# Performance work log

Measured on AMD Instinct MI355X. Metric: run time of the kernel, lower is better.

## Reference

```python
import jax, jax.numpy as jnp
import numpy as np

N = 100000; E = 1600000
X_DIM = 128; Y_DIM = 32; H_DIM = 128; R_DIM = 128; Z_DIM = 64
TAU = 1.0; KEEP = 0.1  # dropout p=0.9 -> keep prob 0.1


def spmm(edge_index, edge_weight, h):
    # out[row] += w * h[col]  (sparse [N,N] @ dense [N,D])
    row, col = edge_index[0], edge_index[1]
    return jax.ops.segment_sum(h[col] * edge_weight[:, None], row, num_segments=N)


def setup_inputs() -> dict:
    key = jax.random.key(0)
    ks = jax.random.split(key, 32)
    p = lambda k, shp: (0.02 * jax.random.normal(k, shp)).astype(jnp.float32)
    inp = {
        'x': jax.random.normal(ks[0], (N, X_DIM), dtype=jnp.float32),
        'y_': jax.random.uniform(ks[1], (N, Y_DIM), dtype=jnp.float32),
        'edge_index': jax.random.randint(ks[2], (2, E), 0, N, dtype=jnp.int32),
        'edge_weight': jax.random.uniform(ks[3], (E,), dtype=jnp.float32),
        'non_label': jax.random.bernoulli(ks[4], 0.5, (N,)),
        # inverted dropout mask, torch semantics: keep w.p. 0.1, scale by 1/0.1
        'dropout_mask': (jax.random.bernoulli(ks[5], KEEP, (N, X_DIM)).astype(jnp.float32) / KEEP),
        'u_gumbel': jax.random.uniform(ks[6], (N, Y_DIM), dtype=jnp.float32),
        'z_eps': jax.random.normal(ks[7], (Z_DIM,), dtype=jnp.float32),
        # x_to_yu (2-layer spmm GCN)
        'Wg1': p(ks[8], (X_DIM, H_DIM)), 'bg1': jnp.zeros((H_DIM,), jnp.float32),
        'Wg2': p(ks[9], (H_DIM, Y_DIM)), 'bg2': jnp.zeros((Y_DIM,), jnp.float32),
        # GSNN_Encoder
        'W_xy': p(ks[10], (H_DIM + Y_DIM, R_DIM)), 'b_xy': jnp.zeros((R_DIM,), jnp.float32),
        'W_hr': p(ks[11], (R_DIM, R_DIM)), 'b_hr': jnp.zeros((R_DIM,), jnp.float32),
        # R_to_MuSigma
        'W_rh': p(ks[12], (R_DIM, R_DIM)), 'b_rh': jnp.zeros((R_DIM,), jnp.float32),
        'W_mu': p(ks[13], (R_DIM, Z_DIM)), 'b_mu': jnp.zeros((Z_DIM,), jnp.float32),
        'W_sig': p(ks[14], (R_DIM, Z_DIM)), 'b_sig': jnp.zeros((Z_DIM,), jnp.float32),
        # GSNN_Decoder
        'W_xh': p(ks[15], (X_DIM, H_DIM)), 'b_xh': jnp.zeros((H_DIM,), jnp.float32),
        'W_h2': p(ks[16], (H_DIM + Z_DIM, H_DIM + Z_DIM)), 'b_h2': jnp.zeros((H_DIM + Z_DIM,), jnp.float32),
        'W_hy': p(ks[17], (H_DIM + Z_DIM, Y_DIM)), 'b_hy': jnp.zeros((Y_DIM,), jnp.float32),
    }
    return inp


def reference(x, y_, edge_index, edge_weight, non_label, dropout_mask, u_gumbel, z_eps,
              Wg1, bg1, Wg2, bg2, W_xy, b_xy, W_hr, b_hr,
              W_rh, b_rh, W_mu, b_mu, W_sig, b_sig,
              W_xh, b_xh, W_h2, b_h2, W_hy, b_hy):
    # ---- x_to_yu: 2-layer spmm GCN -> (y_encode [N,Y], y_embedding [N,H]) ----
    h_emb = jax.nn.relu(spmm(edge_index, edge_weight, x) @ Wg1 + bg1)
    y_encode = spmm(edge_index, edge_weight, h_emb) @ Wg2 + bg2
    # ---- gumbel_softmax(hard=True, tau=1) at non-labelled nodes ----
    g = -jnp.log(-jnp.log(u_gumbel + 1e-10) + 1e-10)
    soft = jax.nn.softmax((y_encode + g) / TAU, axis=-1)
    hard = jax.nn.one_hot(jnp.argmax(soft, axis=-1), Y_DIM, dtype=soft.dtype)
    y_gumbel = hard + soft - jax.lax.stop_gradient(soft)  # straight-through
    y = jnp.where(non_label[:, None], y_gumbel, y_)
    # ---- GSNN_Encoder (adj unused, matching original) ----
    h_enc = jax.nn.relu(jnp.concatenate([h_emb, y], axis=1) @ W_xy + b_xy)
    r_nodes = h_enc @ W_hr + b_hr
    r_graph = jnp.mean(r_nodes, axis=0)  # readout [R]
    # ---- R_to_MuSigma + rsample ----
    hr = jax.nn.relu(r_graph @ W_rh + b_rh)
    mu = hr @ W_mu + b_mu
    sigma = 0.1 + 0.9 * jax.nn.sigmoid(hr @ W_sig + b_sig)
    z = mu + sigma * z_eps  # Normal.rsample
    # ---- GSNN_Decoder ----
    xd = x * dropout_mask
    h = jax.nn.relu(xd @ W_xh + b_xh)
    h = jnp.concatenate([h, jnp.broadcast_to(z, (h.shape[0], Z_DIM))], axis=1)
    h = h / (jnp.linalg.norm(h, axis=1, keepdims=True) + 1e-06)
    h = jax.nn.relu(spmm(edge_index, edge_weight, h) @ W_h2 + b_h2)
    y_pred = spmm(edge_index, edge_weight, h) @ W_hy + b_hy
    return y_pred
```

## Files before the change

kernel.cpp:

```cpp
#include <hip/hip_runtime.h>
#include <hip/hip_bf16.h>

#define NN 100000
#define EE 1600000

typedef unsigned short u16;
typedef unsigned int   u32;
typedef short short8 __attribute__((ext_vector_type(8)));
typedef float v4f    __attribute__((ext_vector_type(4)));
typedef u32 u32x2    __attribute__((ext_vector_type(2)));

__device__ __forceinline__ float b2f(u16 h){ u32 u = ((u32)h) << 16; return __builtin_bit_cast(float, u); }
__device__ __forceinline__ float lo2f(u32 u){ return __builtin_bit_cast(float, u << 16); }
__device__ __forceinline__ float hi2f(u32 u){ return __builtin_bit_cast(float, u & 0xffff0000u); }
__device__ __forceinline__ u16   f2b(float f){ __hip_bfloat16 h = __float2bfloat16(f); return __builtin_bit_cast(u16, h); }
__device__ __forceinline__ float ldx(const void* p, long i, int fm){
  return fm ? ((const float*)p)[i] : b2f(((const u16*)p)[i]);
}
__device__ __forceinline__ float i2f(int v){ return __builtin_bit_cast(float, v); }

__global__ void k_detect(const void* __restrict__ x, const void* __restrict__ nonlab,
                         int* __restrict__ flags){
  __shared__ int s_bad, s_ni, s_nf, s_nb;
  int t = threadIdx.x;
  if (t == 0){ s_bad = 0; s_ni = 0; s_nf = 0; s_nb = 0; }
  __syncthreads();
  u32 w = ((const u32*)x)[t];
  u32 lo = w & 0xffffu, ex = (lo >> 7) & 0xffu;
  if (lo != 0u && (ex < 100u || ex > 140u)) atomicAdd(&s_bad, 1);
  if (t < 64){
    u32 v = ((const u32*)nonlab)[t];
    if (v > 1u) atomicAdd(&s_ni, 1);
    if (v != 0u && v != 0x3F800000u) atomicAdd(&s_nf, 1);
  }
  if (t < 128){
    u16 h = ((const u16*)nonlab)[t];
    if (h != 0 && h != 0x3F80) atomicAdd(&s_nb, 1);
  }
  __syncthreads();
  if (t == 0){
    flags[0] = (s_bad > 32) ? 1 : 0;
    flags[1] = (s_ni == 0) ? 1 : ((s_nf == 0) ? 3 : ((s_nb == 0) ? 2 : 0));
  }
}

#define PW_G1 0
#define PW_G2 16384
#define PW_XY 20480
#define PW_XH 40960
#define PW_H2 57344
#define PW_HY 94208
#define PW_TOT 100352
#define PB_G1 0
#define PB_XY 128
#define PB_XH 256
#define PB_H2 384
#define PB_ZERO 576
#define PB_HY 704
#define PB_TOT 736

__global__ __launch_bounds__(256) void k_pack(const void* W0, const void* W1, const void* W2,
                      const void* W3, const void* W4, const void* W5,
                      const void* b0, const void* b1, const void* b2, const void* b3, const void* b4,
                      u16* __restrict__ Wp, float* __restrict__ bp, const int* __restrict__ flags){
  int e = blockIdx.x * 256 + threadIdx.x;
  int fm = flags[0];
  if (e < PW_TOT){
    const void* src; int off, DOUT;
    if      (e < PW_G2){ src = W0; off = PW_G1; DOUT = 128; }
    else if (e < PW_XY){ src = W1; off = PW_G2; DOUT = 32; }
    else if (e < PW_XH){ src = W2; off = PW_XY; DOUT = 128; }
    else if (e < PW_H2){ src = W3; off = PW_XH; DOUT = 128; }
    else if (e < PW_HY){ src = W4; off = PW_H2; DOUT = 192; }
    else               { src = W5; off = PW_HY; DOUT = 32; }
    int local = e - off;
    int k = local / DOUT, col = local - k * DOUT;
    u16 v = fm ? f2b(((const float*)src)[local]) : ((const u16*)src)[local];
    Wp[off + ((k >> 3) * DOUT + col) * 8 + (k & 7)] = v;
  }
  int eb = e - PW_TOT;
  if (eb >= 0 && eb < PB_TOT){
    float v = 0.f;
    if      (eb < 128) v = ldx(b0, eb, fm);
    else if (eb < 256) v = ldx(b1, eb - 128, fm);
    else if (eb < 384) v = ldx(b2, eb - 256, fm);
    else if (eb < 576) v = ldx(b3, eb - 384, fm);
    else if (eb < 704) v = 0.f;
    else               v = ldx(b4, eb - 704, fm);
    bp[eb] = v;
  }
}

#define BSH 9
#define NBK 196
#define CAP 16384

__global__ __launch_bounds__(256) void k_binA(const int* __restrict__ ei, const void* __restrict__ ew,
                      int* __restrict__ bcnt, int2* __restrict__ stage,
                      const int* __restrict__ flags){
  __shared__ int lcnt[NBK];
  __shared__ int lbase[NBK];
  int t = threadIdx.x;
  for (int i = t; i < NBK; i += 256) lcnt[i] = 0;
  __syncthreads();
  int fm = flags[0];
  long e0 = (long)blockIdx.x * 4096;
  int bb[16], ord[16], pk[16], wb[16];
  #pragma unroll
  for (int j = 0; j < 16; ++j){
    long e = e0 + j * 256 + t;
    bool v = e < EE;
    int r = v ? ei[e] : 0;
    int c = v ? ei[EE + e] : 0;
    float w = v ? ldx(ew, e, fm) : 0.f;
    int b = r >> BSH;
    bb[j] = v ? b : -1;
    pk[j] = ((r & 511) << 17) | c;
    wb[j] = __builtin_bit_cast(int, w);
    if (v) ord[j] = atomicAdd(&lcnt[b], 1);
  }
  __syncthreads();
  for (int i = t; i < NBK; i += 256){
    int c = lcnt[i];
    lbase[i] = c ? atomicAdd(&bcnt[i], c) : 0;
  }
  __syncthreads();
  #pragma unroll
  for (int j = 0; j < 16; ++j){
    if (bb[j] >= 0){
      int pos = lbase[bb[j]] + ord[j];
      if (pos < CAP) stage[(long)bb[j] * CAP + pos] = make_int2(pk[j], wb[j]);
    }
  }
}

__global__ void k_scanB(const int* __restrict__ bcnt, int* __restrict__ bbase,
                        int* __restrict__ rowptr){
  __shared__ int l[256];
  int t = threadIdx.x;
  int v = (t < NBK) ? bcnt[t] : 0;
  l[t] = v; __syncthreads();
  for (int o = 1; o < 256; o <<= 1){
    int x = (t >= o) ? l[t - o] : 0; __syncthreads();
    l[t] += x; __syncthreads();
  }
  if (t < NBK) bbase[t] = l[t] - v;
  if (t == 0) rowptr[NN] = EE;
}

__global__ __launch_bounds__(512) void k_binB(const int* __restrict__ bbase, const int* __restrict__ bcnt,
                      const int2* __restrict__ stage, int2* __restrict__ cpk,
                      int* __restrict__ rowptr){
  __shared__ int cnt[512];
  __shared__ int cur[512];
  int b = blockIdx.x, t = threadIdx.x;
  int r0 = b << BSH;
  int rows = min(512, NN - r0);
  cnt[t] = 0; __syncthreads();
  int cb = min(bcnt[b], CAP);
  const int2* sb = stage + (long)b * CAP;
  for (int j = t; j < cb; j += 512)
    atomicAdd(&cnt[((u32)sb[j].x) >> 17], 1);
  __syncthreads();
  int v = cnt[t];
  cur[t] = v; __syncthreads();
  for (int o = 1; o < 512; o <<= 1){
    int x = (t >= o) ? cur[t - o] : 0; __syncthreads();
    cur[t] += x; __syncthreads();
  }
  int excl = bbase[b] + cur[t] - v;
  if (t < rows) rowptr[r0 + t] = excl;
  __syncthreads();
  cur[t] = excl;
  __syncthreads();
  for (int j = t; j < cb; j += 512){
    int2 w = sb[j];
    int rib = ((u32)w.x) >> 17;
    int pos = atomicAdd(&cur[rib], 1);
    cpk[pos] = make_int2(w.x & 0x1FFFF, w.y);
  }
}

template<bool AG, bool EPI>
__global__ __launch_bounds__(256) void k_spmm(const u16* __restrict__ in, u16* __restrict__ out,
                       const int* __restrict__ rowptr, const int2* __restrict__ cpk,
                       const float* __restrict__ agt, float* __restrict__ agg,
                       const float* __restrict__ bias){
  int wid  = blockIdx.x * 4 + (threadIdx.x >> 6);
  int lane = threadIdx.x & 63;
  if (wid >= NN) return;
  int half = lane >> 5, l16 = lane & 31;
  int s = rowptr[wid], e = rowptr[wid + 1];
  float a0 = 0.f, a1 = 0.f, a2 = 0.f, a3 = 0.f, aga = 0.f;
  for (int j = s; j < e; j += 8){
    int2 pe[4];
    if (j + 8 <= e){
      #pragma unroll
      for (int k = 0; k < 4; ++k) pe[k] = cpk[j + 2 * k + half];
    } else {
      #pragma unroll
      for (int k = 0; k < 4; ++k){
        int idx = j + 2 * k + half;
        int2 w = cpk[idx < e ? idx : j];
        if (idx >= e) w.y = 0;
        pe[k] = w;
      }
    }
    u32x2 u[4];
    #pragma unroll
    for (int k = 0; k < 4; ++k)
      u[k] = *(const u32x2*)(in + (long)pe[k].x * 128 + 4 * l16);
    if (AG && l16 == 0){
      #pragma unroll
      for (int k = 0; k < 4; ++k) aga = fmaf(i2f(pe[k].y), agt[pe[k].x], aga);
    }
    #pragma unroll
    for (int k = 0; k < 4; ++k){
      float wt = i2f(pe[k].y);
      a0 = fmaf(wt, lo2f(u[k].x), a0);
      a1 = fmaf(wt, hi2f(u[k].x), a1);
      a2 = fmaf(wt, lo2f(u[k].y), a2);
      a3 = fmaf(wt, hi2f(u[k].y), a3);
    }
  }
  a0 += __shfl_xor(a0, 32); a1 += __shfl_xor(a1, 32);
  a2 += __shfl_xor(a2, 32); a3 += __shfl_xor(a3, 32);
  if (AG) aga += __shfl_xor(aga, 32);
  if (EPI){
    a0 = fmaxf(a0 + bias[4 * l16],     0.f);
    a1 = fmaxf(a1 + bias[4 * l16 + 1], 0.f);
    a2 = fmaxf(a2 + bias[4 * l16 + 2], 0.f);
    a3 = fmaxf(a3 + bias[4 * l16 + 3], 0.f);
  }
  if (half == 0){
    u32x2 w;
    w.x = (u32)f2b(a0) | ((u32)f2b(a1) << 16);
    w.y = (u32)f2b(a2) | ((u32)f2b(a3) << 16);
    *(u32x2*)(out + (long)wid * 128 + 4 * l16) = w;
    if (AG && l16 == 0) agg[wid] = aga;
  }
}

__global__ __launch_bounds__(256) void k_spmm32b(const u16* __restrict__ in, void* __restrict__ out,
                       const int* __restrict__ rowptr, const int2* __restrict__ cpk,
                       const int* __restrict__ flags, const float* __restrict__ bp){
  int row = blockIdx.x * 16 + (threadIdx.x >> 4);
  int d = threadIdx.x & 15;
  if (row >= NN) return;
  int eh = d >> 3, d8 = d & 7;
  int fm = flags[0];
  int s = rowptr[row], e = rowptr[row + 1];
  float a0 = 0.f, a1 = 0.f, a2 = 0.f, a3 = 0.f;
  for (int j = s; j < e; j += 8){
    int2 p[4];
    if (j + 8 <= e){
      #pragma unroll
      for (int k = 0; k < 4; ++k) p[k] = cpk[j + 2 * k + eh];
    } else {
      #pragma unroll
      for (int k = 0; k < 4; ++k){
        int idx = j + 2 * k + eh;
        int2 w = cpk[idx < e ? idx : j];
        if (idx >= e) w.y = 0;
        p[k] = w;
      }
    }
    u32x2 u[4];
    #pragma unroll
    for (int k = 0; k < 4; ++k) u[k] = *(const u32x2*)(in + (long)p[k].x * 32 + 4 * d8);
    #pragma unroll
    for (int k = 0; k < 4; ++k){
      float wt = i2f(p[k].y);
      a0 = fmaf(wt, lo2f(u[k].x), a0);
      a1 = fmaf(wt, hi2f(u[k].x), a1);
      a2 = fmaf(wt, lo2f(u[k].y), a2);
      a3 = fmaf(wt, hi2f(u[k].y), a3);
    }
  }
  a0 += __shfl_xor(a0, 8); a1 += __shfl_xor(a1, 8);
  a2 += __shfl_xor(a2, 8); a3 += __shfl_xor(a3, 8);
  a0 += bp[4 * d8]; a1 += bp[4 * d8 + 1]; a2 += bp[4 * d8 + 2]; a3 += bp[4 * d8 + 3];
  if (eh == 0){
    if (fm){
      float4 w = make_float4(a0, a1, a2, a3);
      *(float4*)((float*)out + (long)row * 32 + 4 * d8) = w;
    } else {
      u32x2 w;
      w.x = (u32)f2b(a0) | ((u32)f2b(a1) << 16);
      w.y = (u32)f2b(a2) | ((u32)f2b(a3) << 16);
      *(u32x2*)((u16*)out + (long)row * 32 + 4 * d8) = w;
    }
  }
}

__global__ __launch_bounds__(256) void k_spmmg(const u16* __restrict__ in, u16* __restrict__ y,
                       const int* __restrict__ rowptr, const int2* __restrict__ cpk,
                       const int* __restrict__ flags, const void* __restrict__ bg2,
                       const void* __restrict__ ug, const void* __restrict__ ylab,
                       const void* __restrict__ nonlab){
  int row = blockIdx.x * 16 + (threadIdx.x >> 4);
  int d = threadIdx.x & 15;
  if (row >= NN) return;
  int fm = flags[0], mode = flags[1];
  bool nl;
  if      (mode == 1) nl = ((const int*)nonlab)[row] != 0;
  else if (mode == 3) nl = ((const float*)nonlab)[row] != 0.f;
  else if (mode == 2) nl = ((const u16*)nonlab)[row] != 0;
  else                nl = ((const unsigned char*)nonlab)[row] != 0;
  long base = (long)row * 32;
  if (!nl){
    u32 lo, hi;
    if (fm){
      lo = (u32)f2b(((const float*)ylab)[base + 2 * d]);
      hi = (u32)f2b(((const float*)ylab)[base + 2 * d + 1]);
    } else {
      lo = ((const u16*)ylab)[base + 2 * d];
      hi = ((const u16*)ylab)[base + 2 * d + 1];
    }
    *(u32*)(y + base + 2 * d) = lo | (hi << 16);
    return;
  }
  int s = rowptr[row], e = rowptr[row + 1];
  float a0 = 0.f, a1 = 0.f;
  for (int j = s; j < e; j += 8){
    int2 p[8];
    if (j + 8 <= e){
      #pragma unroll
      for (int q = 0; q < 8; ++q) p[q] = cpk[j + q];
    } else {
      #pragma unroll
      for (int q = 0; q < 8; ++q){
        int idx = j + q;
        int2 w = cpk[idx < e ? idx : j];
        if (idx >= e) w.y = 0;
        p[q] = w;
      }
    }
    u32 u[8];
    #pragma unroll
    for (int q = 0; q < 8; ++q) u[q] = *(const u32*)(in + (long)p[q].x * 32 + 2 * d);
    #pragma unroll
    for (int q = 0; q < 8; ++q){
      float wt = i2f(p[q].y);
      a0 = fmaf(wt, lo2f(u[q]), a0); a1 = fmaf(wt, hi2f(u[q]), a1);
    }
  }
  float u0 = ldx(ug, base + 2 * d,     fm);
  float u1 = ldx(ug, base + 2 * d + 1, fm);
  float g0 = -logf(-logf(u0 + 1e-10f) + 1e-10f);
  float g1 = -logf(-logf(u1 + 1e-10f) + 1e-10f);
  float v0 = a0 + ldx(bg2, 2 * d,     fm) + g0;
  float v1 = a1 + ldx(bg2, 2 * d + 1, fm) + g1;
  float bm; int bi;
  if (v0 >= v1){ bm = v0; bi = 2 * d; } else { bm = v1; bi = 2 * d + 1; }
  #pragma unroll
  for (int o = 1; o < 16; o <<= 1){
    float om = __shfl_xor(bm, o);
    int   oi = __shfl_xor(bi, o);
    if (om > bm || (om == bm && oi < bi)){ bm = om; bi = oi; }
  }
  u32 lo = (2 * d     == bi) ? 0x3F80u : 0u;
  u32 hi = (2 * d + 1 == bi) ? 0x3F80u : 0u;
  *(u32*)(y + base + 2 * d) = lo | (hi << 16);
}

template<int K, int DOUT, int CT, int RTW, bool RELU, int AMODE, int OMODE, bool CSUM>
__global__ __launch_bounds__(256) void k_mm(const u16* __restrict__ A, const void* __restrict__ A2,
     const void* __restrict__ A3, const u16* __restrict__ Wp, const float* __restrict__ bp,
     void* __restrict__ outv, const int* __restrict__ flags, float* __restrict__ csacc){
  constexpr int STEPS = K / 32;
  constexpr int G = DOUT / (16 * CT);
  constexpr int CHUNKS = 6250 / RTW;
  __shared__ float lsum[128];
  int wid = blockIdx.x * 4 + (threadIdx.x >> 6);
  if (wid >= G * CHUNKS) return;
  int g = wid % G; long chunk = wid / G;
  int lane = threadIdx.x & 63, n = lane & 15, q = lane >> 4;
  int colOff = g * CT * 16;
  int fm = (AMODE == 4) ? flags[0] : 0;

  if (CSUM){
    if (threadIdx.x < 128) lsum[threadIdx.x] = 0.f;
    __syncthreads();
  }

  short8 B[CT][STEPS];
  float bv[CT];
  #pragma unroll
  for (int ct = 0; ct < CT; ++ct){
    int col = colOff + ct * 16 + n;
    bv[ct] = bp[col];
    #pragma unroll
    for (int s = 0; s < STEPS; ++s)
      B[ct][s] = *(const short8*)(Wp + (((s * 4 + q) * DOUT) + col) * 8);
  }

  float csum[CT];
  #pragma unroll
  for (int ct = 0; ct < CT; ++ct) csum[ct] = 0.f;

  for (int rt = 0; rt < RTW; ++rt){
    long rowbase = (chunk * RTW + rt) * 16;
    long arow = rowbase + n;
    v4f acc[CT] = {};
    #pragma unroll
    for (int s = 0; s < STEPS; ++s){
      short8 a;
      if (AMODE == 0){
        a = *(const short8*)(A + arow * K + s * 32 + q * 8);
      } else if (AMODE == 2){
        if (s < 4) a = *(const short8*)(A + arow * 128 + s * 32 + q * 8);
        else       a = *(const short8*)((const u16*)A2 + arow * 32 + q * 8);
      } else {
        long base = arow * 128 + s * 32 + q * 8;
        if (fm){
          const float* xp = (const float*)A2 + base;
          float4 x0 = *(const float4*)xp, x1 = *(const float4*)(xp + 4);
          a[0] = (short)f2b(x0.x); a[1] = (short)f2b(x0.y);
          a[2] = (short)f2b(x0.z); a[3] = (short)f2b(x0.w);
          a[4] = (short)f2b(x1.x); a[5] = (short)f2b(x1.y);
          a[6] = (short)f2b(x1.z); a[7] = (short)f2b(x1.w);
        } else {
          a = *(const short8*)((const u16*)A2 + base);
        }
      }
      #pragma unroll
      for (int ct = 0; ct < CT; ++ct)
        acc[ct] = __builtin_amdgcn_mfma_f32_16x16x32_bf16(a, B[ct][s], acc[ct], 0, 0, 0);
    }
    long orow = rowbase + q * 4;
    #pragma unroll
    for (int ct = 0; ct < CT; ++ct){
      int col = colOff + ct * 16 + n;
      #pragma unroll
      for (int r = 0; r < 4; ++r){
        float v = acc[ct][r] + bv[ct];
        if (RELU) v = fmaxf(v, 0.f);
        if (CSUM) csum[ct] += v;
        if (OMODE != 3){
          long oi = (orow + r) * (long)DOUT + col;
          if (OMODE == 2) ((float*)outv)[oi] = v;
          else            ((u16*)outv)[oi] = f2b(v);
        }
      }
    }
  }
  if (CSUM){
    #pragma unroll
    for (int ct = 0; ct < CT; ++ct){
      csum[ct] += __shfl_xor(csum[ct], 16);
      csum[ct] += __shfl_xor(csum[ct], 32);
      if (lane < 16) atomicAdd(&lsum[colOff + ct * 16 + n], csum[ct]);
    }
    __syncthreads();
    if (threadIdx.x < 128) csacc[(long)blockIdx.x * 128 + threadIdx.x] = lsum[threadIdx.x];
  }
}

__global__ __launch_bounds__(256) void k_mmh2(const u16* __restrict__ A, const float* __restrict__ AG2,
     const float* __restrict__ zbuf, const u16* __restrict__ Wh2p, const float* __restrict__ bh2p,
     const u16* __restrict__ Whyp, u16* __restrict__ tbuf){
  __shared__ u16 hl[16][200];
  int w = threadIdx.x >> 6;
  int lane = threadIdx.x & 63, n = lane & 15, q = lane >> 4;
  int colOff = w * 48;

  short8 B[3][6];
  float bv[3];
  #pragma unroll
  for (int ct = 0; ct < 3; ++ct){
    int col = colOff + ct * 16 + n;
    bv[ct] = bh2p[col];
    #pragma unroll
    for (int s = 0; s < 6; ++s)
      B[ct][s] = *(const short8*)(Wh2p + (((s * 4 + q) * 192) + col) * 8);
  }
  short8 B2[2][6];
  if (w == 0){
    #pragma unroll
    for (int ct = 0; ct < 2; ++ct){
      int col = ct * 16 + n;
      #pragma unroll
      for (int s = 0; s < 6; ++s)
        B2[ct][s] = *(const short8*)(Whyp + (((s * 4 + q) * 32) + col) * 8);
    }
  }

  for (int rt = 0; rt < 2; ++rt){
    long rowbase = ((long)blockIdx.x * 2 + rt) * 16;
    long arow = rowbase + n;
    float agr = AG2[arow];
    v4f acc[3] = {};
    #pragma unroll
    for (int s = 0; s < 6; ++s){
      short8 a;
      if (s < 4) a = *(const short8*)(A + arow * 128 + s * 32 + q * 8);
      else {
        #pragma unroll
        for (int j = 0; j < 8; ++j) a[j] = (short)f2b(agr * zbuf[(s - 4) * 32 + q * 8 + j]);
      }
      #pragma unroll
      for (int ct = 0; ct < 3; ++ct)
        acc[ct] = __builtin_amdgcn_mfma_f32_16x16x32_bf16(a, B[ct][s], acc[ct], 0, 0, 0);
    }
    #pragma unroll
    for (int ct = 0; ct < 3; ++ct){
      int col = colOff + ct * 16 + n;
      #pragma unroll
      for (int r = 0; r < 4; ++r)
        hl[q * 4 + r][col] = f2b(fmaxf(acc[ct][r] + bv[ct], 0.f));
    }
    __syncthreads();
    if (w == 0){
      v4f a2[2] = {};
      #pragma unroll
      for (int s = 0; s < 6; ++s){
        short8 a = *(const short8*)(&hl[n][s * 32 + q * 8]);
        #pragma unroll
        for (int ct = 0; ct < 2; ++ct)
          a2[ct] = __builtin_amdgcn_mfma_f32_16x16x32_bf16(a, B2[ct][s], a2[ct], 0, 0, 0);
      }
      #pragma unroll
      for (int ct = 0; ct < 2; ++ct){
        int col = ct * 16 + n;
        #pragma unroll
        for (int r = 0; r < 4; ++r)
          tbuf[(rowbase + q * 4 + r) * 32 + col] = f2b(a2[ct][r]);
      }
    }
    __syncthreads();
  }
}

__global__ __launch_bounds__(256) void k_csred(const float* __restrict__ pb, float* __restrict__ accum){
  __shared__ float l[256];
  int c = blockIdx.x, t = threadIdx.x;
  float s = 0.f;
  for (int r = t; r < 1563; r += 256) s += pb[(long)r * 128 + c];
  l[t] = s; __syncthreads();
  for (int o = 128; o; o >>= 1){ if (t < o) l[t] += l[t + o]; __syncthreads(); }
  if (t == 0) accum[c] = l[0];
}

__global__ __launch_bounds__(256) void k_mmnorm(const void* __restrict__ A2, const void* __restrict__ A3,
     const u16* __restrict__ Wp, const float* __restrict__ bp,
     u16* __restrict__ outHs, float* __restrict__ ag,
     const float* __restrict__ zbuf, const int* __restrict__ flags){
  constexpr int STEPS = 4, CT = 8, CHUNKS = 6250;
  int wid = blockIdx.x * 4 + (threadIdx.x >> 6);
  if (wid >= CHUNKS) return;
  long chunk = wid;
  int lane = threadIdx.x & 63, n = lane & 15, q = lane >> 4;
  int fm = flags[0];

  short8 B[CT][STEPS];
  float bv[CT];
  #pragma unroll
  for (int ct = 0; ct < CT; ++ct){
    int col = ct * 16 + n;
    bv[ct] = bp[col];
    #pragma unroll
    for (int s = 0; s < STEPS; ++s)
      B[ct][s] = *(const short8*)(Wp + (((s * 4 + q) * 128) + col) * 8);
  }
  float zz = zbuf[64];

  {
    long rowbase = chunk * 16;
    long arow = rowbase + n;
    v4f acc[CT] = {};
    #pragma unroll
    for (int s = 0; s < STEPS; ++s){
      short8 a;
      long base = arow * 128 + s * 32 + q * 8;
      if (fm){
        const float* xp = (const float*)A2 + base;
        const float* dp = (const float*)A3 + base;
        float4 x0 = *(const float4*)xp, x1 = *(const float4*)(xp + 4);
        float4 d0 = *(const float4*)dp, d1 = *(const float4*)(dp + 4);
        a[0] = (short)f2b(x0.x * d0.x); a[1] = (short)f2b(x0.y * d0.y);
        a[2] = (short)f2b(x0.z * d0.z); a[3] = (short)f2b(x0.w * d0.w);
        a[4] = (short)f2b(x1.x * d1.x); a[5] = (short)f2b(x1.y * d1.y);
        a[6] = (short)f2b(x1.z * d1.z); a[7] = (short)f2b(x1.w * d1.w);
      } else {
        short8 xv = *(const short8*)((const u16*)A2 + base);
        short8 dv = *(const short8*)((const u16*)A3 + base);
        #pragma unroll
        for (int j = 0; j < 8; ++j) a[j] = (short)f2b(b2f((u16)xv[j]) * b2f((u16)dv[j]));
      }
      #pragma unroll
      for (int ct = 0; ct < CT; ++ct)
        acc[ct] = __builtin_amdgcn_mfma_f32_16x16x32_bf16(a, B[ct][s], acc[ct], 0, 0, 0);
    }
    float v[CT][4];
    float sqr[4] = {0.f, 0.f, 0.f, 0.f};
    #pragma unroll
    for (int ct = 0; ct < CT; ++ct){
      #pragma unroll
      for (int r = 0; r < 4; ++r){
        float t = fmaxf(acc[ct][r] + bv[ct], 0.f);
        v[ct][r] = t;
        sqr[r] += t * t;
      }
    }
    #pragma unroll
    for (int r = 0; r < 4; ++r){
      #pragma unroll
      for (int o = 1; o < 16; o <<= 1) sqr[r] += __shfl_xor(sqr[r], o);
    }
    float scale[4];
    #pragma unroll
    for (int r = 0; r < 4; ++r) scale[r] = 1.f / (sqrtf(sqr[r] + zz) + 1e-6f);
    long orow = rowbase + q * 4;
    #pragma unroll
    for (int ct = 0; ct < CT; ++ct){
      int col = ct * 16 + n;
      #pragma unroll
      for (int r = 0; r < 4; ++r)
        outHs[(orow + r) * 128 + col] = f2b(v[ct][r] * scale[r]);
    }
    if (n == 0){
      #pragma unroll
      for (int r = 0; r < 4; ++r) ag[orow + r] = scale[r];
    }
  }
}

__global__ void k_z(const float* __restrict__ accum,
                    const void* Whr, const void* bhr, const void* Wrh, const void* brh,
                    const void* Wmu, const void* bmu, const void* Wsig, const void* bsig,
                    const void* zeps, float* __restrict__ zout, const int* __restrict__ flags){
  __shared__ float hm[128], rg[128], hr[128], zl[64];
  int t = threadIdx.x, fm = flags[0];
  hm[t] = accum[t] * (1.0f / 100000.0f);
  __syncthreads();
  { float s = ldx(bhr, t, fm);
    for (int k = 0; k < 128; ++k) s = fmaf(hm[k], ldx(Whr, (long)k * 128 + t, fm), s);
    rg[t] = s; }
  __syncthreads();
  { float s = ldx(brh, t, fm);
    for (int k = 0; k < 128; ++k) s = fmaf(rg[k], ldx(Wrh, (long)k * 128 + t, fm), s);
    hr[t] = fmaxf(s, 0.f); }
  __syncthreads();
  if (t < 64){
    float m = ldx(bmu, t, fm), sv = ldx(bsig, t, fm);
    for (int k = 0; k < 128; ++k){
      float h = hr[k];
      m  = fmaf(h, ldx(Wmu,  (long)k * 64 + t, fm), m);
      sv = fmaf(h, ldx(Wsig, (long)k * 64 + t, fm), sv);
    }
    float sig = 0.1f + 0.9f / (1.f + expf(-sv));
    float z = fmaf(sig, ldx(zeps, t, fm), m);
    zl[t] = z; zout[t] = z;
  }
  __syncthreads();
  if (t == 0){ float ss = 0.f; for (int j = 0; j < 64; ++j) ss += zl[j] * zl[j]; zout[64] = ss; }
}

extern "C" void kernel_launch(void* const* d_in, const int* in_sizes, int n_in,
                              void* d_out, int out_size, void* d_ws, size_t ws_size,
                              hipStream_t stream){
  const void* x    = d_in[0];
  const void* ylab = d_in[1];
  const int*  ei   = (const int*)d_in[2];
  const void* ew   = d_in[3];
  const void* nonlab = d_in[4];
  const void* dm   = d_in[5];
  const void* ug   = d_in[6];
  const void* zeps = d_in[7];
  const void* Wg1 = d_in[8],  *bg1 = d_in[9];
  const void* Wg2 = d_in[10], *bg2 = d_in[11];
  const void* Wxy = d_in[12], *bxy = d_in[13];
  const void* Whr = d_in[14], *bhr = d_in[15];
  const void* Wrh = d_in[16], *brh = d_in[17];
  const void* Wmu = d_in[18], *bmu = d_in[19];
  const void* Wsg = d_in[20], *bsg = d_in[21];
  const void* Wxh = d_in[22], *bxh = d_in[23];
  const void* Wh2 = d_in[24], *bh2 = d_in[25];
  const void* Why = d_in[26], *bhy = d_in[27];

  char* ws = (char*)d_ws;
  size_t off = 0;
  auto alloc = [&](size_t bytes){ void* p = ws + off; off += (bytes + 511) & ~(size_t)511; return p; };
  int*   flags  = (int*)  alloc(256);
  int*   rowptr = (int*)  alloc((size_t)(NN + 1) * 4);
  int*   bbase  = (int*)  alloc(1024 * 4);
  float* accum  = (float*)alloc(1024 * 4);
  u16*   Wpack  = (u16*)  alloc((size_t)PW_TOT * 2);
  float* bpack  = (float*)alloc((size_t)PB_TOT * 4);
  float* AG1    = (float*)alloc((size_t)NN * 4);
  float* AG2    = (float*)alloc((size_t)NN * 4);
  float* pb     = (float*)alloc((size_t)1563 * 128 * 4);
  int2*  cpk    = (int2*) alloc((size_t)EE * 8);
  u16*   B0     = (u16*)  alloc((size_t)NN * 192 * 2);
  u16*   B1     = (u16*)  alloc((size_t)NN * 192 * 2);
  u16* yproj = B0 + (size_t)NN * 128;
  u16* ybuf  = B1 + (size_t)NN * 160;
  int2* stage = (int2*)B0;
  u16* tbuf = B1;
  int* bcnt = (int*)(accum + 512);

  hipMemsetAsync(accum, 0, 1024 * 4, stream);
  k_detect<<<1, 256, 0, stream>>>(x, nonlab, flags);
  k_pack<<<(PW_TOT + PB_TOT + 255) / 256, 256, 0, stream>>>(Wg1, Wg2, Wxy, Wxh, Wh2, Why,
                                                            bg1, bxy, bxh, bh2, bhy, Wpack, bpack, flags);
  k_binA <<<(EE + 4095) / 4096, 256, 0, stream>>>(ei, ew, bcnt, stage, flags);
  k_scanB<<<1, 256, 0, stream>>>(bcnt, bbase, rowptr);
  k_binB <<<NBK, 512, 0, stream>>>(bbase, bcnt, stage, cpk, rowptr);
  k_mm<128,128,4,2,false,4,0,false><<<1563, 256, 0, stream>>>(nullptr, x, nullptr, Wpack + PW_G1, bpack + PB_ZERO, B1, flags, nullptr);
  k_spmm<false,true ><<<25000, 256, 0, stream>>>(B1, B0, rowptr, cpk, nullptr, nullptr, bpack + PB_G1);
  k_mm<128,32 ,2,1,false,0,0,false><<<1563, 256, 0, stream>>>(B0, nullptr, nullptr, Wpack + PW_G2, bpack + PB_ZERO, yproj, flags, nullptr);
  k_spmmg<<<6250, 256, 0, stream>>>(yproj, ybuf, rowptr, cpk, flags, bg2, ug, ylab, nonlab);
  k_mm<160,128,4,2,true ,2,3,true ><<<1563, 256, 0, stream>>>(B0, ybuf, nullptr, Wpack + PW_XY, bpack + PB_XY, nullptr, flags, pb);
  k_csred<<<128, 256, 0, stream>>>(pb, accum);
  k_z<<<1, 128, 0, stream>>>(accum, Whr, bhr, Wrh, brh, Wmu, bmu, Wsg, bsg, zeps, accum + 128, flags);
  k_mmnorm<<<1563, 256, 0, stream>>>(x, dm, Wpack + PW_XH, bpack + PB_XH, B1, AG1, accum + 128, flags);
  k_spmm<true ,false><<<25000, 256, 0, stream>>>(B1, B0, rowptr, cpk, AG1, AG2, nullptr);
  k_mmh2<<<3125, 256, 0, stream>>>(B0, AG2, accum + 128, Wpack + PW_H2, bpack + PB_H2,
                                   Wpack + PW_HY, tbuf);
  k_spmm32b<<<6250, 256, 0, stream>>>(tbuf, d_out, rowptr, cpk, flags, bpack + PB_HY);
}
```

Before: 580.5 us.

## Fuse x@Wg1 matmul with edge binning kernel; split spmmg edges across half-waves

```diff
diff --git a/kernel.cpp b/kernel.cpp
--- a/kernel.cpp
+++ b/kernel.cpp
@@ -95,41 +95,92 @@
 #define NBK 196
 #define CAP 16384
 
-__global__ __launch_bounds__(256) void k_binA(const int* __restrict__ ei, const void* __restrict__ ew,
-                      int* __restrict__ bcnt, int2* __restrict__ stage,
-                      const int* __restrict__ flags){
-  __shared__ int lcnt[NBK];
-  __shared__ int lbase[NBK];
-  int t = threadIdx.x;
-  for (int i = t; i < NBK; i += 256) lcnt[i] = 0;
-  __syncthreads();
-  int fm = flags[0];
-  long e0 = (long)blockIdx.x * 4096;
-  int bb[16], ord[16], pk[16], wb[16];
-  #pragma unroll
-  for (int j = 0; j < 16; ++j){
-    long e = e0 + j * 256 + t;
-    bool v = e < EE;
-    int r = v ? ei[e] : 0;
-    int c = v ? ei[EE + e] : 0;
-    float w = v ? ldx(ew, e, fm) : 0.f;
-    int b = r >> BSH;
-    bb[j] = v ? b : -1;
-    pk[j] = ((r & 511) << 17) | c;
-    wb[j] = __builtin_bit_cast(int, w);
-    if (v) ord[j] = atomicAdd(&lcnt[b], 1);
-  }
-  __syncthreads();
-  for (int i = t; i < NBK; i += 256){
-    int c = lcnt[i];
-    lbase[i] = c ? atomicAdd(&bcnt[i], c) : 0;
-  }
-  __syncthreads();
-  #pragma unroll
-  for (int j = 0; j < 16; ++j){
-    if (bb[j] >= 0){
-      int pos = lbase[bb[j]] + ord[j];
-      if (pos < CAP) stage[(long)bb[j] * CAP + pos] = make_int2(pk[j], wb[j]);
+__global__ __launch_bounds__(256) void k_front(const void* __restrict__ x,
+     const u16* __restrict__ Wg1p, u16* __restrict__ xpo, const int* __restrict__ flags,
+     const int* __restrict__ ei, const void* __restrict__ ew,
+     int* __restrict__ bcnt, int2* __restrict__ stage){
+  if (blockIdx.x < 1563){
+    constexpr int STEPS = 4, CT = 4, RTW = 2, G = 2;
+    int wid = blockIdx.x * 4 + (threadIdx.x >> 6);
+    if (wid >= 6250) return;
+    int g = wid % G; long chunk = wid / G;
+    int lane = threadIdx.x & 63, n = lane & 15, q = lane >> 4;
+    int colOff = g * 64;
+    int fm = flags[0];
+    short8 B[CT][STEPS];
+    #pragma unroll
+    for (int ct = 0; ct < CT; ++ct){
+      int col = colOff + ct * 16 + n;
+      #pragma unroll
+      for (int s = 0; s < STEPS; ++s)
+        B[ct][s] = *(const short8*)(Wg1p + (((s * 4 + q) * 128) + col) * 8);
+    }
+    for (int rt = 0; rt < RTW; ++rt){
+      long rowbase = (chunk * RTW + rt) * 16;
+      long arow = rowbase + n;
+      v4f acc[CT] = {};
+      #pragma unroll
+      for (int s = 0; s < STEPS; ++s){
+        short8 a;
+        long base = arow * 128 + s * 32 + q * 8;
+        if (fm){
+          const float* xp = (const float*)x + base;
+          float4 x0 = *(const float4*)xp, x1 = *(const float4*)(xp + 4);
+          a[0] = (short)f2b(x0.x); a[1] = (short)f2b(x0.y);
+          a[2] = (short)f2b(x0.z); a[3] = (short)f2b(x0.w);
+          a[4] = (short)f2b(x1.x); a[5] = (short)f2b(x1.y);
+          a[6] = (short)f2b(x1.z); a[7] = (short)f2b(x1.w);
+        } else {
+          a = *(const short8*)((const u16*)x + base);
+        }
+        #pragma unroll
+        for (int ct = 0; ct < CT; ++ct)
+          acc[ct] = __builtin_amdgcn_mfma_f32_16x16x32_bf16(a, B[ct][s], acc[ct], 0, 0, 0);
+      }
+      long orow = rowbase + q * 4;
+      #pragma unroll
+      for (int ct = 0; ct < CT; ++ct){
+        int col = colOff + ct * 16 + n;
+        #pragma unroll
+        for (int r = 0; r < 4; ++r)
+          xpo[(orow + r) * 128 + col] = f2b(acc[ct][r]);
+      }
+    }
+  } else {
+    __shared__ int lcnt[NBK];
+    __shared__ int lbase[NBK];
+    int t = threadIdx.x;
+    int bid = blockIdx.x - 1563;
+    for (int i = t; i < NBK; i += 256) lcnt[i] = 0;
+    __syncthreads();
+    int fm = flags[0];
+    long e0 = (long)bid * 4096;
+    int bb[16], ord[16], pk[16], wb[16];
+    #pragma unroll
+    for (int j = 0; j < 16; ++j){
+      long e = e0 + j * 256 + t;
+      bool v = e < EE;
+      int r = v ? ei[e] : 0;
+      int c = v ? ei[EE + e] : 0;
+      float w = v ? ldx(ew, e, fm) : 0.f;
+      int b = r >> BSH;
+      bb[j] = v ? b : -1;
+      pk[j] = ((r & 511) << 17) | c;
+      wb[j] = __builtin_bit_cast(int, w);
+      if (v) ord[j] = atomicAdd(&lcnt[b], 1);
+    }
+    __syncthreads();
+    for (int i = t; i < NBK; i += 256){
+      int c = lcnt[i];
+      lbase[i] = c ? atomicAdd(&bcnt[i], c) : 0;
+    }
+    __syncthreads();
+    #pragma unroll
+    for (int j = 0; j < 16; ++j){
+      if (bb[j] >= 0){
+        int pos = lbase[bb[j]] + ord[j];
+        if (pos < CAP) stage[(long)bb[j] * CAP + pos] = make_int2(pk[j], wb[j]);
+      }
     }
   }
 }
@@ -320,48 +371,59 @@
     *(u32*)(y + base + 2 * d) = lo | (hi << 16);
     return;
   }
+  int eh = d >> 3, d8 = d & 7;
   int s = rowptr[row], e = rowptr[row + 1];
-  float a0 = 0.f, a1 = 0.f;
+  float a0 = 0.f, a1 = 0.f, a2 = 0.f, a3 = 0.f;
   for (int j = s; j < e; j += 8){
-    int2 p[8];
+    int2 p[4];
     if (j + 8 <= e){
       #pragma unroll
-      for (int q = 0; q < 8; ++q) p[q] = cpk[j + q];
+      for (int k = 0; k < 4; ++k) p[k] = cpk[j + 2 * k + eh];
     } else {
       #pragma unroll
-      for (int q = 0; q < 8; ++q){
-        int idx = j + q;
+      for (int k = 0; k < 4; ++k){
+        int idx = j + 2 * k + eh;
         int2 w = cpk[idx < e ? idx : j];
         if (idx >= e) w.y = 0;
-        p[q] = w;
-      }
-    }
-    u32 u[8];
-    #pragma unroll
-    for (int q = 0; q < 8; ++q) u[q] = *(const u32*)(in + (long)p[q].x * 32 + 2 * d);
-    #pragma unroll
-    for (int q = 0; q < 8; ++q){
-      float wt = i2f(p[q].y);
-      a0 = fmaf(wt, lo2f(u[q]), a0); a1 = fmaf(wt, hi2f(u[q]), a1);
-    }
-  }
-  float u0 = ldx(ug, base + 2 * d,     fm);
-  float u1 = ldx(ug, base + 2 * d + 1, fm);
-  float g0 = -logf(-logf(u0 + 1e-10f) + 1e-10f);
-  float g1 = -logf(-logf(u1 + 1e-10f) + 1e-10f);
-  float v0 = a0 + ldx(bg2, 2 * d,     fm) + g0;
-  float v1 = a1 + ldx(bg2, 2 * d + 1, fm) + g1;
-  float bm; int bi;
-  if (v0 >= v1){ bm = v0; bi = 2 * d; } else { bm = v1; bi = 2 * d + 1; }
+        p[k] = w;
+      }
+    }
+    u32x2 u[4];
+    #pragma unroll
+    for (int k = 0; k < 4; ++k) u[k] = *(const u32x2*)(in + (long)p[k].x * 32 + 4 * d8);
+    #pragma unroll
+    for (int k = 0; k < 4; ++k){
+      float wt = i2f(p[k].y);
+      a0 = fmaf(wt, lo2f(u[k].x), a0);
+      a1 = fmaf(wt, hi2f(u[k].x), a1);
+      a2 = fmaf(wt, lo2f(u[k].y), a2);
+      a3 = fmaf(wt, hi2f(u[k].y), a3);
+    }
+  }
+  a0 += __shfl_xor(a0, 8); a1 += __shfl_xor(a1, 8);
+  a2 += __shfl_xor(a2, 8); a3 += __shfl_xor(a3, 8);
+  float av[4] = {a0, a1, a2, a3};
+  int c0 = 4 * d8;
+  float bm = -1e30f; int bi = 0;
+  #pragma unroll
+  for (int jj = 0; jj < 4; ++jj){
+    float uu = ldx(ug, base + c0 + jj, fm);
+    float g = -logf(-logf(uu + 1e-10f) + 1e-10f);
+    float v = av[jj] + ldx(bg2, c0 + jj, fm) + g;
+    if (v > bm){ bm = v; bi = c0 + jj; }
+  }
   #pragma unroll
   for (int o = 1; o < 16; o <<= 1){
     float om = __shfl_xor(bm, o);
     int   oi = __shfl_xor(bi, o);
     if (om > bm || (om == bm && oi < bi)){ bm = om; bi = oi; }
   }
-  u32 lo = (2 * d     == bi) ? 0x3F80u : 0u;
-  u32 hi = (2 * d + 1 == bi) ? 0x3F80u : 0u;
-  *(u32*)(y + base + 2 * d) = lo | (hi << 16);
+  if (eh == 0){
+    u32x2 w;
+    w.x = ((c0     == bi) ? 0x3F80u : 0u) | (((c0 + 1 == bi) ? 0x3F80u : 0u) << 16);
+    w.y = ((c0 + 2 == bi) ? 0x3F80u : 0u) | (((c0 + 3 == bi) ? 0x3F80u : 0u) << 16);
+    *(u32x2*)(y + base + c0) = w;
+  }
 }
 
 template<int K, int DOUT, int CT, int RTW, bool RELU, int AMODE, int OMODE, bool CSUM>
@@ -377,7 +439,6 @@
   int g = wid % G; long chunk = wid / G;
   int lane = threadIdx.x & 63, n = lane & 15, q = lane >> 4;
   int colOff = g * CT * 16;
-  int fm = (AMODE == 4) ? flags[0] : 0;
 
   if (CSUM){
     if (threadIdx.x < 128) lsum[threadIdx.x] = 0.f;
@@ -408,21 +469,9 @@
       short8 a;
       if (AMODE == 0){
         a = *(const short8*)(A + arow * K + s * 32 + q * 8);
-      } else if (AMODE == 2){
+      } else {
         if (s < 4) a = *(const short8*)(A + arow * 128 + s * 32 + q * 8);
         else       a = *(const short8*)((const u16*)A2 + arow * 32 + q * 8);
-      } else {
-        long base = arow * 128 + s * 32 + q * 8;
-        if (fm){
-          const float* xp = (const float*)A2 + base;
-          float4 x0 = *(const float4*)xp, x1 = *(const float4*)(xp + 4);
-          a[0] = (short)f2b(x0.x); a[1] = (short)f2b(x0.y);
-          a[2] = (short)f2b(x0.z); a[3] = (short)f2b(x0.w);
-          a[4] = (short)f2b(x1.x); a[5] = (short)f2b(x1.y);
-          a[6] = (short)f2b(x1.z); a[7] = (short)f2b(x1.w);
-        } else {
-          a = *(const short8*)((const u16*)A2 + base);
-        }
       }
       #pragma unroll
       for (int ct = 0; ct < CT; ++ct)
@@ -439,8 +488,7 @@
         if (CSUM) csum[ct] += v;
         if (OMODE != 3){
           long oi = (orow + r) * (long)DOUT + col;
-          if (OMODE == 2) ((float*)outv)[oi] = v;
-          else            ((u16*)outv)[oi] = f2b(v);
+          ((u16*)outv)[oi] = f2b(v);
         }
       }
     }
@@ -704,10 +752,9 @@
   k_detect<<<1, 256, 0, stream>>>(x, nonlab, flags);
   k_pack<<<(PW_TOT + PB_TOT + 255) / 256, 256, 0, stream>>>(Wg1, Wg2, Wxy, Wxh, Wh2, Why,
                                                             bg1, bxy, bxh, bh2, bhy, Wpack, bpack, flags);
-  k_binA <<<(EE + 4095) / 4096, 256, 0, stream>>>(ei, ew, bcnt, stage, flags);
+  k_front<<<1954, 256, 0, stream>>>(x, Wpack + PW_G1, B1, flags, ei, ew, bcnt, stage);
   k_scanB<<<1, 256, 0, stream>>>(bcnt, bbase, rowptr);
   k_binB <<<NBK, 512, 0, stream>>>(bbase, bcnt, stage, cpk, rowptr);
-  k_mm<128,128,4,2,false,4,0,false><<<1563, 256, 0, stream>>>(nullptr, x, nullptr, Wpack + PW_G1, bpack + PB_ZERO, B1, flags, nullptr);
   k_spmm<false,true ><<<25000, 256, 0, stream>>>(B1, B0, rowptr, cpk, nullptr, nullptr, bpack + PB_G1);
   k_mm<128,32 ,2,1,false,0,0,false><<<1563, 256, 0, stream>>>(B0, nullptr, nullptr, Wpack + PW_G2, bpack + PB_ZERO, yproj, flags, nullptr);
   k_spmmg<<<6250, 256, 0, stream>>>(yproj, ybuf, rowptr, cpk, flags, bg2, ug, ylab, nonlab);
```

After: 571.6 us. No clear change (-1.5%).
